# Kernel tuning notes

Hardware: AMD Instinct MI355X
Metric: run time of the kernel (lower is better)

Reference implementation:

```python
import jax, jax.numpy as jnp
import numpy as np

B, N, C, H = 16, 800, 1024, 16
NC = 128  # cached KV length from the N==128 pass
HD = C // H


def setup_inputs() -> dict:
    key = jax.random.key(0)
    ks = jax.random.split(key, 9)
    s = 0.02  # init scale for weights
    return {
        "x": jax.random.normal(ks[0], (B, N, C), jnp.float32),
        "xpos": jax.random.normal(ks[1], (B, N, C), jnp.float32),
        "k_t": jax.random.normal(ks[2], (B, NC, C), jnp.float32),
        "v_t": jax.random.normal(ks[3], (B, NC, C), jnp.float32),
        "Wq": jax.random.normal(ks[4], (C, C), jnp.float32) * s,
        "Wk": jax.random.normal(ks[5], (C, C), jnp.float32) * s,
        "Wv": jax.random.normal(ks[6], (C, C), jnp.float32) * s,
        "Wp": jax.random.normal(ks[7], (C, C), jnp.float32) * s,
        "bp": jnp.zeros((C,), jnp.float32),
    }


def reference(x, xpos, k_t, v_t, Wq, Wk, Wv, Wp, bp):
    # N == 800 branch: q from x+xpos; k/v concat cached k_t/v_t before projection.
    b, n, c = x.shape
    scale = HD ** -0.5

    q = (x + xpos) @ Wq.T                              # [B, N, C]
    k_in = jnp.concatenate([x + xpos, k_t], axis=1)    # [B, N+NC, C]
    v_in = jnp.concatenate([x, v_t], axis=1)           # [B, N+NC, C]
    k = k_in @ Wk.T
    v = v_in @ Wv.T

    def heads(t):
        return t.reshape(b, t.shape[1], H, HD).transpose(0, 2, 1, 3)  # [B,H,L,HD]

    qh, kh, vh = heads(q), heads(k), heads(v)
    attn = jax.nn.softmax(jnp.einsum('bhqd,bhkd->bhqk', qh, kh) * scale, axis=-1)
    out = jnp.einsum('bhqk,bhkd->bhqd', attn, vh)       # [B,H,N,HD]
    out = out.transpose(0, 2, 1, 3).reshape(b, n, c)
    return out @ Wp.T + bp
```

## Files before the change

### kernel.cpp

```cpp
#include <hip/hip_runtime.h>
#include <hip/hip_bf16.h>

#define NB 16
#define NN 800
#define NCACHE 128
#define NL 928
#define CC 1024
#define NH 16
#define HD 64

typedef __attribute__((ext_vector_type(8))) short bf16x8;
typedef __attribute__((ext_vector_type(4))) float f32x4;
typedef __attribute__((ext_vector_type(2))) __bf16 bf2;

__device__ __forceinline__ short f2bf(float x) {
  union { float f; unsigned u; } c; c.f = x;
  unsigned r = c.u + 0x7fffu + ((c.u >> 16) & 1u);
  return (short)(r >> 16);
}

#define GLD_LDS(gp, lp) __builtin_amdgcn_global_load_lds( \
    (__attribute__((address_space(1))) void*)(gp),        \
    (__attribute__((address_space(3))) void*)(lp), 16, 0, 0)

__global__ __launch_bounds__(256) void prep_kv(
    const float* __restrict__ x, const float* __restrict__ xpos,
    const float* __restrict__ ktc, const float* __restrict__ vtc,
    short* __restrict__ k_in, short* __restrict__ v_in) {
  int idx = blockIdx.x * 256 + threadIdx.x;
  int chunk = idx & 127;
  int row = idx >> 7;
  int b = row / NL;
  int lr = row - b * NL;
  int c = chunk * 8;
  float vk[8], vv[8];
  if (lr < NN) {
    const float4* px = (const float4*)(x + ((size_t)(b * NN + lr) * CC + c));
    const float4* pp = (const float4*)(xpos + ((size_t)(b * NN + lr) * CC + c));
    float4 x0 = px[0], x1 = px[1], p0 = pp[0], p1 = pp[1];
    vv[0]=x0.x; vv[1]=x0.y; vv[2]=x0.z; vv[3]=x0.w;
    vv[4]=x1.x; vv[5]=x1.y; vv[6]=x1.z; vv[7]=x1.w;
    vk[0]=x0.x+p0.x; vk[1]=x0.y+p0.y; vk[2]=x0.z+p0.z; vk[3]=x0.w+p0.w;
    vk[4]=x1.x+p1.x; vk[5]=x1.y+p1.y; vk[6]=x1.z+p1.z; vk[7]=x1.w+p1.w;
  } else {
    const float4* pk = (const float4*)(ktc + ((size_t)(b * NCACHE + lr - NN) * CC + c));
    const float4* pv = (const float4*)(vtc + ((size_t)(b * NCACHE + lr - NN) * CC + c));
    float4 k0 = pk[0], k1 = pk[1], v0 = pv[0], v1 = pv[1];
    vk[0]=k0.x; vk[1]=k0.y; vk[2]=k0.z; vk[3]=k0.w;
    vk[4]=k1.x; vk[5]=k1.y; vk[6]=k1.z; vk[7]=k1.w;
    vv[0]=v0.x; vv[1]=v0.y; vv[2]=v0.z; vv[3]=v0.w;
    vv[4]=v1.x; vv[5]=v1.y; vv[6]=v1.z; vv[7]=v1.w;
  }
  bf16x8 ok, ov;
#pragma unroll
  for (int i = 0; i < 8; ++i) { ok[i] = f2bf(vk[i]); ov[i] = f2bf(vv[i]); }
  *(bf16x8*)(k_in + (size_t)row * CC + c) = ok;
  *(bf16x8*)(v_in + (size_t)row * CC + c) = ov;
}

__global__ __launch_bounds__(256) void prep_w(
    const float* __restrict__ Wq, const float* __restrict__ Wk,
    const float* __restrict__ Wv, const float* __restrict__ Wp,
    short* __restrict__ wout) {
  int idx = blockIdx.x * 256 + threadIdx.x;
  int wsel = idx >> 17;
  int off = (idx & 131071) * 8;
  const float* src = wsel == 0 ? Wq : wsel == 1 ? Wk : wsel == 2 ? Wv : Wp;
  float sc = wsel == 0 ? 0.18033688011112042f : 1.0f;
  const float4* p = (const float4*)(src + off);
  float4 a = p[0], b = p[1];
  bf16x8 o;
  o[0]=f2bf(a.x*sc); o[1]=f2bf(a.y*sc); o[2]=f2bf(a.z*sc); o[3]=f2bf(a.w*sc);
  o[4]=f2bf(b.x*sc); o[5]=f2bf(b.y*sc); o[6]=f2bf(b.z*sc); o[7]=f2bf(b.w*sc);
  *(bf16x8*)(wout + (size_t)wsel * 1048576 + off) = o;
}

template<int MODE>
__global__ __launch_bounds__(256) void gemm_bt(
    const short* __restrict__ A, const short* __restrict__ Bw,
    short* __restrict__ o0, short* __restrict__ o1,
    float* __restrict__ of, const float* __restrict__ bias) {
  __shared__ short As[128 * 32];
  __shared__ short Bs[128 * 32];
  const int tid = threadIdx.x;
  const int l = tid & 63;
  const int w = tid >> 6;
  const int wr = w >> 1, wc = w & 1;
  const int lr = l & 15, g = l >> 4;
  const int cpx = gridDim.x >> 3;
  const int swz = (blockIdx.x & 7) * cpx + (blockIdx.x >> 3);
  int bm, bn;
  if (MODE == 2) { bm = swz >> 4; bn = swz & 15; }
  else           { bm = swz >> 3; bn = swz & 7; }
  const int m0 = bm * 128, n0 = bn * 128;

  const int ch0 = tid, ch1 = tid + 256;
  const short* pa0 = A + (size_t)(m0 + (ch0 >> 2)) * CC + (ch0 & 3) * 8;
  const short* pa1 = A + (size_t)(m0 + (ch1 >> 2)) * CC + (ch1 & 3) * 8;
  const short* pb0 = Bw + (size_t)(n0 + (ch0 >> 2)) * CC + (ch0 & 3) * 8;
  const short* pb1 = Bw + (size_t)(n0 + (ch1 >> 2)) * CC + (ch1 & 3) * 8;
  short* la0 = As + ch0 * 8; short* la1 = As + ch1 * 8;
  short* lb0 = Bs + ch0 * 8; short* lb1 = Bs + ch1 * 8;

  f32x4 acc[4][4] = {};

  for (int kk = 0; kk < CC; kk += 32) {
    GLD_LDS(pa0 + kk, la0);
    GLD_LDS(pa1 + kk, la1);
    GLD_LDS(pb0 + kk, lb0);
    GLD_LDS(pb1 + kk, lb1);
    __syncthreads();
    bf16x8 af[4], bfv[4];
#pragma unroll
    for (int i = 0; i < 4; ++i)
      af[i] = *(const bf16x8*)(As + (wr * 64 + i * 16 + lr) * 32 + g * 8);
#pragma unroll
    for (int n = 0; n < 4; ++n)
      bfv[n] = *(const bf16x8*)(Bs + (wc * 64 + n * 16 + lr) * 32 + g * 8);
#pragma unroll
    for (int i = 0; i < 4; ++i)
#pragma unroll
      for (int n = 0; n < 4; ++n)
        acc[i][n] = __builtin_amdgcn_mfma_f32_16x16x32_bf16(af[i], bfv[n], acc[i][n], 0, 0, 0);
    __syncthreads();
  }

#pragma unroll
  for (int i = 0; i < 4; ++i)
#pragma unroll
    for (int n = 0; n < 4; ++n) {
      if (MODE == 1) {
        const int col = n0 + wc * 64 + n * 16 + lr;
        const float bv = bias[col];
#pragma unroll
        for (int j = 0; j < 4; ++j) {
          const int row = m0 + wr * 64 + i * 16 + g * 4 + j;
          of[(size_t)row * CC + col] = acc[i][n][j] + bv;
        }
      } else if (MODE == 2) {
        short* base = (bn < 8) ? o0 : o1;
        const int col = (bn & 7) * 128 + wc * 64 + n * 16 + lr;
#pragma unroll
        for (int j = 0; j < 4; ++j) {
          const int row = m0 + wr * 64 + i * 16 + g * 4 + j;
          base[(size_t)row * CC + col] = f2bf(acc[i][n][j]);
        }
      } else {
        const int col = n0 + wc * 64 + n * 16 + lr;
        const int r0 = m0 + wr * 64 + i * 16 + g * 4;
        const int b = r0 / NL;
        const int rb = r0 - b * NL;
        const int vtrow = (b * NH + (col >> 6)) * HD + (col & 63);
        ushort4 pk4;
        pk4.x = (unsigned short)f2bf(acc[i][n][0]);
        pk4.y = (unsigned short)f2bf(acc[i][n][1]);
        pk4.z = (unsigned short)f2bf(acc[i][n][2]);
        pk4.w = (unsigned short)f2bf(acc[i][n][3]);
        *(ushort4*)(o0 + (size_t)vtrow * NL + rb) = pk4;
      }
    }
}

__global__ __launch_bounds__(256, 4) void attn_fwd(
    const short* __restrict__ qb, const short* __restrict__ kbuf,
    const short* __restrict__ vtb, short* __restrict__ ob) {
  __shared__ short smem[2][4096];
  const int tid = threadIdx.x;
  const int w = tid >> 6;
  const int l = tid & 63;
  const int c = l & 15, g = l >> 4;
  const int swzb = (blockIdx.x & 7) * 224 + (blockIdx.x >> 3);
  const int bh = swzb / 7;
  const int blk7 = swzb - bh * 7;
  const int h = bh & 15, b = bh >> 4;
  const int q0 = blk7 * 128 + w * 32;
  const bool active = q0 < NN;

  const int u = l >> 3;
  const int lK = 8 * w + u;
  const int b16 = lK & 15;
  const int rpK = 8 * (b16 >> 2) + (b16 & 3) + 4 * (lK >> 4);
  const int xK = (l & 7) ^ u;
  const short* srcK = kbuf + (size_t)b * NL * CC + (size_t)rpK * CC + h * HD + xK * 8;
  const int dV = 16 * w + (l >> 2);
  const int xV = (l & 3) ^ ((l >> 3) & 3);
  const short* srcV = vtb + (size_t)bh * HD * NL + (size_t)dV * NL + xV * 8;

  bf16x8 qf[2][2];
  if (active) {
#pragma unroll
    for (int f = 0; f < 2; ++f) {
      const short* qrow = qb + ((size_t)(b * NL + q0 + f * 16 + c) * CC + h * HD + g * 8);
      qf[f][0] = *(const bf16x8*)qrow;
      qf[f][1] = *(const bf16x8*)(qrow + 32);
    }
  }

  const int koff0 = c * 64 + ((g ^ (c & 7)) << 3);
  const int koff1 = c * 64 + (((g + 4) ^ (c & 7)) << 3);
  const int voffb = 2048 + c * 32 + ((g ^ ((c >> 1) & 3)) << 3);

  f32x4 acc[2][4] = {};
  f32x4 ellv[2] = {};

  GLD_LDS(srcK, &smem[0][w * 512]);
  GLD_LDS(srcV, &smem[0][2048 + w * 512]);
  __syncthreads();

  int buf = 0;
  for (int t = 0; t < 29; ++t) {
    if (t < 28) {
      GLD_LDS(srcK + (size_t)(t + 1) * 32 * CC, &smem[buf ^ 1][w * 512]);
      GLD_LDS(srcV + (t + 1) * 32, &smem[buf ^ 1][2048 + w * 512]);
    }
    if (active) {
      const short* S = smem[buf];
      bf16x8 kd0 = *(const bf16x8*)(S + koff0);
      bf16x8 kd1 = *(const bf16x8*)(S + koff1);
      bf16x8 kd2 = *(const bf16x8*)(S + koff0 + 1024);
      bf16x8 kd3 = *(const bf16x8*)(S + koff1 + 1024);
      bf16x8 vf0 = *(const bf16x8*)(S + voffb);
      bf16x8 vf1 = *(const bf16x8*)(S + voffb + 512);
      bf16x8 vf2 = *(const bf16x8*)(S + voffb + 1024);
      bf16x8 vf3 = *(const bf16x8*)(S + voffb + 1536);
      __builtin_amdgcn_s_setprio(1);
#pragma unroll
      for (int f = 0; f < 2; ++f) {
        f32x4 z = {0.f, 0.f, 0.f, 0.f};
        f32x4 s0 = __builtin_amdgcn_mfma_f32_16x16x32_bf16(kd0, qf[f][0], z, 0, 0, 0);
        s0 = __builtin_amdgcn_mfma_f32_16x16x32_bf16(kd1, qf[f][1], s0, 0, 0, 0);
        f32x4 s1 = __builtin_amdgcn_mfma_f32_16x16x32_bf16(kd2, qf[f][0], z, 0, 0, 0);
        s1 = __builtin_amdgcn_mfma_f32_16x16x32_bf16(kd3, qf[f][1], s1, 0, 0, 0);
        f32x4 e0, e1;
        e0[0] = __builtin_amdgcn_exp2f(s0[0]);
        e0[1] = __builtin_amdgcn_exp2f(s0[1]);
        e0[2] = __builtin_amdgcn_exp2f(s0[2]);
        e0[3] = __builtin_amdgcn_exp2f(s0[3]);
        e1[0] = __builtin_amdgcn_exp2f(s1[0]);
        e1[1] = __builtin_amdgcn_exp2f(s1[1]);
        e1[2] = __builtin_amdgcn_exp2f(s1[2]);
        e1[3] = __builtin_amdgcn_exp2f(s1[3]);
        ellv[f] += e0 + e1;
        union { bf2 h2[4]; bf16x8 v; } pu;
        pu.h2[0] = bf2{(__bf16)e0[0], (__bf16)e0[1]};
        pu.h2[1] = bf2{(__bf16)e0[2], (__bf16)e0[3]};
        pu.h2[2] = bf2{(__bf16)e1[0], (__bf16)e1[1]};
        pu.h2[3] = bf2{(__bf16)e1[2], (__bf16)e1[3]};
        acc[f][0] = __builtin_amdgcn_mfma_f32_16x16x32_bf16(pu.v, vf0, acc[f][0], 0, 0, 0);
        acc[f][1] = __builtin_amdgcn_mfma_f32_16x16x32_bf16(pu.v, vf1, acc[f][1], 0, 0, 0);
        acc[f][2] = __builtin_amdgcn_mfma_f32_16x16x32_bf16(pu.v, vf2, acc[f][2], 0, 0, 0);
        acc[f][3] = __builtin_amdgcn_mfma_f32_16x16x32_bf16(pu.v, vf3, acc[f][3], 0, 0, 0);
      }
      __builtin_amdgcn_s_setprio(0);
    }
    __syncthreads();
    buf ^= 1;
  }

  if (active) {
    float rinv[2];
#pragma unroll
    for (int f = 0; f < 2; ++f) {
      float e = (ellv[f][0] + ellv[f][1]) + (ellv[f][2] + ellv[f][3]);
      e += __shfl_xor(e, 16);
      e += __shfl_xor(e, 32);
      rinv[f] = 1.0f / e;
    }
#pragma unroll
    for (int f = 0; f < 2; ++f) {
      float rj[4];
#pragma unroll
      for (int j = 0; j < 4; ++j) rj[j] = __shfl(rinv[f], g * 4 + j);
      short* orow = ob + (size_t)(b * NN + q0 + f * 16 + g * 4) * CC + h * HD + c;
#pragma unroll
      for (int n = 0; n < 4; ++n)
#pragma unroll
        for (int j = 0; j < 4; ++j)
          orow[(size_t)j * CC + n * 16] = f2bf(acc[f][n][j] * rj[j]);
    }
  }
}

extern "C" void kernel_launch(void* const* d_in, const int* in_sizes, int n_in,
                              void* d_out, int out_size, void* d_ws, size_t ws_size,
                              hipStream_t stream) {
  const float* x    = (const float*)d_in[0];
  const float* xpos = (const float*)d_in[1];
  const float* k_t  = (const float*)d_in[2];
  const float* v_t  = (const float*)d_in[3];
  const float* Wq   = (const float*)d_in[4];
  const float* Wk   = (const float*)d_in[5];
  const float* Wv   = (const float*)d_in[6];
  const float* Wp   = (const float*)d_in[7];
  const float* bp   = (const float*)d_in[8];
  float* out = (float*)d_out;

  char* ws = (char*)d_ws;
  short* k_in = (short*)ws;
  short* v_in = (short*)(ws + 30408704);
  short* wqb  = (short*)(ws + 60817408);
  short* wvb  = (short*)(ws + 65011712);
  short* wpb  = (short*)(ws + 67108864);
  short* qbuf = (short*)(ws + 69206016);
  short* kbuf = (short*)(ws + 99614720);
  short* vtb  = (short*)(ws + 130023424);
  short* attn_o = k_in;

  prep_kv<<<7424, 256, 0, stream>>>(x, xpos, k_t, v_t, k_in, v_in);
  prep_w<<<2048, 256, 0, stream>>>(Wq, Wk, Wv, Wp, wqb);
  gemm_bt<2><<<1856, 256, 0, stream>>>(k_in, wqb, qbuf, kbuf, nullptr, nullptr);
  gemm_bt<3><<<928, 256, 0, stream>>>(v_in, wvb, vtb, nullptr, nullptr, nullptr);
  attn_fwd<<<1792, 256, 0, stream>>>(qbuf, kbuf, vtb, attn_o);
  gemm_bt<1><<<800, 256, 0, stream>>>(attn_o, wpb, nullptr, nullptr, out, bp);
}
```

Measured before the change: 278.4 us.

## Replace 128x128 GEMM with 256x256 double-buffered swizzled-LDS 8-wave GEMM

```diff
diff --git a/kernel.cpp b/kernel.cpp
--- a/kernel.cpp
+++ b/kernel.cpp
@@ -22,6 +22,9 @@
 #define GLD_LDS(gp, lp) __builtin_amdgcn_global_load_lds( \
     (__attribute__((address_space(1))) void*)(gp),        \
     (__attribute__((address_space(3))) void*)(lp), 16, 0, 0)
+
+#define BAR() asm volatile("s_barrier" ::: "memory")
+#define SCHEDB() __builtin_amdgcn_sched_barrier(0)
 
 __global__ __launch_bounds__(256) void prep_kv(
     const float* __restrict__ x, const float* __restrict__ xpos,
@@ -75,87 +78,140 @@
   *(bf16x8*)(wout + (size_t)wsel * 1048576 + off) = o;
 }
 
+#define READ_A(QR) \
+  _Pragma("unroll") \
+  for (int fr = 0; fr < 4; ++fr) \
+    _Pragma("unroll") \
+    for (int ks = 0; ks < 2; ++ks) \
+      af[fr][ks] = *(const bf16x8*)&lds[abase + (QR)*4096 + fr*1024 + (ks ? xk1 : xk0)];
+
+#define READ_B(QC) \
+  _Pragma("unroll") \
+  for (int fc = 0; fc < 2; ++fc) \
+    _Pragma("unroll") \
+    for (int ks = 0; ks < 2; ++ks) \
+      bfv[(QC)*2+fc][ks] = *(const bf16x8*)&lds[bbase + (QC)*2048 + fc*1024 + (ks ? xk1 : xk0)];
+
+#define MFMA_QUAD(QR, QC) \
+  SCHEDB(); __builtin_amdgcn_s_setprio(1); \
+  _Pragma("unroll") \
+  for (int fr = 0; fr < 4; ++fr) \
+    _Pragma("unroll") \
+    for (int fc = 0; fc < 2; ++fc) \
+      _Pragma("unroll") \
+      for (int ks = 0; ks < 2; ++ks) \
+        acc[(QR)*4+fr][(QC)*2+fc] = __builtin_amdgcn_mfma_f32_16x16x32_bf16( \
+            af[fr][ks], bfv[(QC)*2+fc][ks], acc[(QR)*4+fr][(QC)*2+fc], 0, 0, 0); \
+  __builtin_amdgcn_s_setprio(0); SCHEDB()
+
 template<int MODE>
-__global__ __launch_bounds__(256) void gemm_bt(
+__global__ __launch_bounds__(512, 2) void gemm256(
     const short* __restrict__ A, const short* __restrict__ Bw,
     short* __restrict__ o0, short* __restrict__ o1,
     float* __restrict__ of, const float* __restrict__ bias) {
-  __shared__ short As[128 * 32];
-  __shared__ short Bs[128 * 32];
+  __shared__ short lds[65536];
   const int tid = threadIdx.x;
-  const int l = tid & 63;
-  const int w = tid >> 6;
-  const int wr = w >> 1, wc = w & 1;
-  const int lr = l & 15, g = l >> 4;
+  const int w = tid >> 6, l = tid & 63;
+  const int wm = w >> 2, wn = w & 3;
+  const int c = l & 15, g2 = l >> 4;
+  const int BNT = (MODE == 2) ? 8 : 4;
   const int cpx = gridDim.x >> 3;
   const int swz = (blockIdx.x & 7) * cpx + (blockIdx.x >> 3);
-  int bm, bn;
-  if (MODE == 2) { bm = swz >> 4; bn = swz & 15; }
-  else           { bm = swz >> 3; bn = swz & 7; }
-  const int m0 = bm * 128, n0 = bn * 128;
-
-  const int ch0 = tid, ch1 = tid + 256;
-  const short* pa0 = A + (size_t)(m0 + (ch0 >> 2)) * CC + (ch0 & 3) * 8;
-  const short* pa1 = A + (size_t)(m0 + (ch1 >> 2)) * CC + (ch1 & 3) * 8;
-  const short* pb0 = Bw + (size_t)(n0 + (ch0 >> 2)) * CC + (ch0 & 3) * 8;
-  const short* pb1 = Bw + (size_t)(n0 + (ch1 >> 2)) * CC + (ch1 & 3) * 8;
-  short* la0 = As + ch0 * 8; short* la1 = As + ch1 * 8;
-  short* lb0 = Bs + ch0 * 8; short* lb1 = Bs + ch1 * 8;
-
-  f32x4 acc[4][4] = {};
-
-  for (int kk = 0; kk < CC; kk += 32) {
-    GLD_LDS(pa0 + kk, la0);
-    GLD_LDS(pa1 + kk, la1);
-    GLD_LDS(pb0 + kk, lb0);
-    GLD_LDS(pb1 + kk, lb1);
-    __syncthreads();
-    bf16x8 af[4], bfv[4];
-#pragma unroll
-    for (int i = 0; i < 4; ++i)
-      af[i] = *(const bf16x8*)(As + (wr * 64 + i * 16 + lr) * 32 + g * 8);
-#pragma unroll
-    for (int n = 0; n < 4; ++n)
-      bfv[n] = *(const bf16x8*)(Bs + (wc * 64 + n * 16 + lr) * 32 + g * 8);
-#pragma unroll
-    for (int i = 0; i < 4; ++i)
-#pragma unroll
-      for (int n = 0; n < 4; ++n)
-        acc[i][n] = __builtin_amdgcn_mfma_f32_16x16x32_bf16(af[i], bfv[n], acc[i][n], 0, 0, 0);
-    __syncthreads();
-  }
-
-#pragma unroll
-  for (int i = 0; i < 4; ++i)
-#pragma unroll
-    for (int n = 0; n < 4; ++n) {
+  const int bm = swz / BNT, bn = swz % BNT;
+  const int m0 = bm * 256, n0 = bn * 256;
+
+  const int R0 = tid >> 3;
+  const int gc0 = (tid & 7) ^ (R0 & 7);
+  const short* As_ = A + (size_t)(m0 + R0) * CC + gc0 * 8;
+  const short* Bs_ = Bw + (size_t)(n0 + R0) * CC + gc0 * 8;
+  const int wofs = w * 512;
+
+#define STAGE_HT(slot, src) do { \
+    GLD_LDS((src), &lds[(slot) + wofs]); \
+    GLD_LDS((src) + 64 * CC, &lds[(slot) + 4096 + wofs]); } while (0)
+
+  const int xk0 = ((g2) ^ (c & 7)) * 8;
+  const int xk1 = ((g2 + 4) ^ (c & 7)) * 8;
+
+  f32x4 acc[8][4] = {};
+
+  STAGE_HT(0,        As_);
+  STAGE_HT(8192,     As_ + 128 * CC);
+  STAGE_HT(16384,    Bs_);
+  STAGE_HT(24576,    Bs_ + 128 * CC);
+  STAGE_HT(32768,       As_ + 64);
+  STAGE_HT(32768+8192,  As_ + 64 + 128 * CC);
+  STAGE_HT(32768+16384, Bs_ + 64);
+  STAGE_HT(32768+24576, Bs_ + 64 + 128 * CC);
+  asm volatile("s_waitcnt vmcnt(8)" ::: "memory");
+  BAR();
+
+#pragma unroll 1
+  for (int t = 0; t < 16; ++t) {
+    const int pb = (t & 1) << 15;
+    const int abase = pb + wm * 8192 + c * 64;
+    const int bbase = pb + 16384 + ((wn >> 1) << 13) + ((wn & 1) * 64 + c) * 64;
+    bf16x8 af[4][2], bfv[4][2];
+    READ_A(0);
+    READ_B(0);
+    BAR();
+    MFMA_QUAD(0, 0);
+    BAR();
+    READ_B(1);
+    BAR();
+    MFMA_QUAD(0, 1);
+    BAR();
+    READ_A(1);
+    if (t < 14) {
+      const short* bs2 = Bs_ + (t + 2) * 64;
+      STAGE_HT(pb + 16384, bs2);
+      STAGE_HT(pb + 24576, bs2 + 128 * CC);
+    }
+    BAR();
+    MFMA_QUAD(1, 0);
+    BAR();
+    if (t < 14) {
+      const short* as2 = As_ + (t + 2) * 64;
+      STAGE_HT(pb, as2);
+      STAGE_HT(pb + 8192, as2 + 128 * CC);
+      asm volatile("s_waitcnt vmcnt(8)" ::: "memory");
+    } else if (t == 14) {
+      asm volatile("s_waitcnt vmcnt(0)" ::: "memory");
+    }
+    BAR();
+    MFMA_QUAD(1, 1);
+    BAR();
+  }
+
+#pragma unroll
+  for (int fr = 0; fr < 8; ++fr)
+#pragma unroll
+    for (int fc = 0; fc < 4; ++fc) {
+      const int row = m0 + wm * 128 + fr * 16 + g2 * 4;
+      const int colw = wn * 64 + fc * 16 + c;
       if (MODE == 1) {
-        const int col = n0 + wc * 64 + n * 16 + lr;
+        const int col = n0 + colw;
         const float bv = bias[col];
 #pragma unroll
-        for (int j = 0; j < 4; ++j) {
-          const int row = m0 + wr * 64 + i * 16 + g * 4 + j;
-          of[(size_t)row * CC + col] = acc[i][n][j] + bv;
-        }
+        for (int j = 0; j < 4; ++j)
+          of[(size_t)(row + j) * CC + col] = acc[fr][fc][j] + bv;
       } else if (MODE == 2) {
-        short* base = (bn < 8) ? o0 : o1;
-        const int col = (bn & 7) * 128 + wc * 64 + n * 16 + lr;
-#pragma unroll
-        for (int j = 0; j < 4; ++j) {
-          const int row = m0 + wr * 64 + i * 16 + g * 4 + j;
-          base[(size_t)row * CC + col] = f2bf(acc[i][n][j]);
-        }
+        const int col2 = n0 + colw;
+        short* base = (col2 < 1024) ? o0 : o1;
+        const int col = col2 & 1023;
+#pragma unroll
+        for (int j = 0; j < 4; ++j)
+          base[(size_t)(row + j) * CC + col] = f2bf(acc[fr][fc][j]);
       } else {
-        const int col = n0 + wc * 64 + n * 16 + lr;
-        const int r0 = m0 + wr * 64 + i * 16 + g * 4;
-        const int b = r0 / NL;
-        const int rb = r0 - b * NL;
+        const int col = n0 + colw;
+        const int b = row / NL;
+        const int rb = row - b * NL;
         const int vtrow = (b * NH + (col >> 6)) * HD + (col & 63);
         ushort4 pk4;
-        pk4.x = (unsigned short)f2bf(acc[i][n][0]);
-        pk4.y = (unsigned short)f2bf(acc[i][n][1]);
-        pk4.z = (unsigned short)f2bf(acc[i][n][2]);
-        pk4.w = (unsigned short)f2bf(acc[i][n][3]);
+        pk4.x = (unsigned short)f2bf(acc[fr][fc][0]);
+        pk4.y = (unsigned short)f2bf(acc[fr][fc][1]);
+        pk4.z = (unsigned short)f2bf(acc[fr][fc][2]);
+        pk4.w = (unsigned short)f2bf(acc[fr][fc][3]);
         *(ushort4*)(o0 + (size_t)vtrow * NL + rb) = pk4;
       }
     }
@@ -308,8 +364,8 @@
 
   prep_kv<<<7424, 256, 0, stream>>>(x, xpos, k_t, v_t, k_in, v_in);
   prep_w<<<2048, 256, 0, stream>>>(Wq, Wk, Wv, Wp, wqb);
-  gemm_bt<2><<<1856, 256, 0, stream>>>(k_in, wqb, qbuf, kbuf, nullptr, nullptr);
-  gemm_bt<3><<<928, 256, 0, stream>>>(v_in, wvb, vtb, nullptr, nullptr, nullptr);
+  gemm256<2><<<464, 512, 0, stream>>>(k_in, wqb, qbuf, kbuf, nullptr, nullptr);
+  gemm256<3><<<232, 512, 0, stream>>>(v_in, wvb, vtb, nullptr, nullptr, nullptr);
   attn_fwd<<<1792, 256, 0, stream>>>(qbuf, kbuf, vtb, attn_o);
-  gemm_bt<1><<<800, 256, 0, stream>>>(attn_o, wpb, nullptr, nullptr, out, bp);
-}
+  gemm256<1><<<200, 512, 0, stream>>>(attn_o, wpb, nullptr, nullptr, out, bp);
+}
```

After: 248.0 us. -10.9%, faster.
